# Kernel optimization log

Hardware: AMD Instinct MI355X
Metric: run time of the kernel (lower is better)

## Reference

```python
import jax, jax.numpy as jnp
import numpy as np

B, S, D = 2, 2048, 1024
H, DH = 16, 64  # num_heads, per-head depth (kd//H == vd//H)
NEG = -1e10


def setup_inputs() -> dict:
    key = jax.random.key(0)
    ks = jax.random.split(key, 5)
    scale = 0.02
    return {
        "X": jax.random.normal(ks[0], (B, S, D), dtype=jnp.float32),
        "Wq": jax.random.normal(ks[1], (D, D), dtype=jnp.float32) * scale,
        "Wk": jax.random.normal(ks[2], (D, D), dtype=jnp.float32) * scale,
        "Wv": jax.random.normal(ks[3], (D, D), dtype=jnp.float32) * scale,
        "Wo": jax.random.normal(ks[4], (D, D), dtype=jnp.float32) * scale,
    }


def reference(X, Wq, Wk, Wv, Wo):
    # torch nn.Linear(in,out,bias=False): y = x @ W.T, W is [out,in]
    q = X @ Wq.T  # [B,S,H*DH]
    k = X @ Wk.T
    v = X @ Wv.T
    # split heads -> [B,H,S,DH]
    q = q.reshape(B, S, H, DH).transpose(0, 2, 1, 3) * (DH ** -0.5)
    k = k.reshape(B, S, H, DH).transpose(0, 2, 1, 3)
    v = v.reshape(B, S, H, DH).transpose(0, 2, 1, 3)
    # causal bias: -1e10 on strictly upper triangle (psuedolikelihood=False)
    bias = NEG * jnp.triu(jnp.ones((S, S), dtype=jnp.float32), 1)
    # logits[...,q,k] = q . k
    logits = jnp.einsum("bhkd,bhqd->bhqk", k, q) + bias
    weights = jax.nn.softmax(logits, axis=-1)  # [B,H,S,S]
    out = jnp.einsum("bhqk,bhkd->bhqd", weights, v)
    out = out.transpose(0, 2, 1, 3).reshape(B, S, H * DH)
    return out @ Wo.T  # [B,S,D]
```

## Files before the change

### kernel.cpp

```cpp
#include <hip/hip_runtime.h>
#include <math.h>


typedef _Float16 f16x8 __attribute__((ext_vector_type(8)));
typedef _Float16 f16x4 __attribute__((ext_vector_type(4)));
typedef _Float16 f16x2 __attribute__((ext_vector_type(2)));
typedef __attribute__((ext_vector_type(4))) float f32x4;
typedef __attribute__((ext_vector_type(16))) float f32x16;

#define MFMA16(a, b, c) __builtin_amdgcn_mfma_f32_16x16x32_f16(a, b, c, 0, 0, 0)
#define MFMA32(a, b, c) __builtin_amdgcn_mfma_f32_32x32x16_f16(a, b, c, 0, 0, 0)
#define QSCALE 0.18033688f

__device__ __forceinline__ void async16(const void* g, void* l) {
  __builtin_amdgcn_global_load_lds(
      (const __attribute__((address_space(1))) unsigned int*)g,
      (__attribute__((address_space(3))) unsigned int*)l, 16, 0, 0);
}

__device__ __forceinline__ f16x2 pk2(float x, float y) {
  return __builtin_bit_cast(f16x2, __builtin_amdgcn_cvt_pkrtz(x, y));
}

__device__ __forceinline__ f16x8 cvt8(const float* __restrict__ p) {
  float4 a = *(const float4*)p;
  float4 b = *(const float4*)(p + 4);
  f16x2 p0 = pk2(a.x, a.y), p1 = pk2(a.z, a.w);
  f16x2 p2 = pk2(b.x, b.y), p3 = pk2(b.z, b.w);
  f16x8 h;
  h[0] = p0[0]; h[1] = p0[1]; h[2] = p1[0]; h[3] = p1[1];
  h[4] = p2[0]; h[5] = p2[1]; h[6] = p3[0]; h[7] = p3[1];
  return h;
}

__global__ void convert_all(const float* __restrict__ X, const float* __restrict__ Wq,
                            const float* __restrict__ Wk, const float* __restrict__ Wv,
                            const float* __restrict__ Wo, _Float16* __restrict__ Xh,
                            _Float16* __restrict__ Wqkvh, _Float16* __restrict__ Woh) {
  size_t i = ((size_t)blockIdx.x * 256 + threadIdx.x) * 8;
  const float* src; _Float16* dst; size_t off;
  if (i < 4194304u)      { src = X;  dst = Xh;              off = i; }
  else if (i < 5242880u) { src = Wq; dst = Wqkvh;           off = i - 4194304u; }
  else if (i < 6291456u) { src = Wk; dst = Wqkvh + 1048576; off = i - 5242880u; }
  else if (i < 7340032u) { src = Wv; dst = Wqkvh + 2097152; off = i - 6291456u; }
  else                   { src = Wo; dst = Woh;             off = i - 7340032u; }
  *(f16x8*)(dst + off) = cvt8(src + off);
}

__global__ __launch_bounds__(256) void gemm_qkv_a(
    const _Float16* __restrict__ Xh, const _Float16* __restrict__ Wh,
    _Float16* __restrict__ Qh, _Float16* __restrict__ Kh,
    _Float16* __restrict__ Vth) {
  __shared__ _Float16 As[128 * 32];
  __shared__ _Float16 Bs[128 * 32];
  const int tid = threadIdx.x;
  const int wave = tid >> 6, lane = tid & 63;
  const int quad = lane >> 4, l16 = lane & 15;
  const int wm = (wave >> 1) * 64, wn = (wave & 1) * 64;
  const int bn = blockIdx.x, bm = blockIdx.y;
  const int mat = bn >> 3;

  const int r0 = tid >> 2, cc0 = (tid & 3) * 8;
  const int r1 = (tid + 256) >> 2, cc1 = (tid & 3) * 8;
  const _Float16* gA0 = &Xh[(size_t)(bm * 128 + r0) * 1024 + cc0];
  const _Float16* gA1 = &Xh[(size_t)(bm * 128 + r1) * 1024 + cc1];
  const _Float16* gB0 = &Wh[(size_t)(bn * 128 + r0) * 1024 + cc0];
  const _Float16* gB1 = &Wh[(size_t)(bn * 128 + r1) * 1024 + cc1];

  f32x4 acc[4][4] = {};

  for (int k0 = 0; k0 < 1024; k0 += 32) {
    __syncthreads();
    async16(gA0 + k0, &As[(wave * 64) * 8]);
    async16(gA1 + k0, &As[(256 + wave * 64) * 8]);
    async16(gB0 + k0, &Bs[(wave * 64) * 8]);
    async16(gB1 + k0, &Bs[(256 + wave * 64) * 8]);
    __syncthreads();
    f16x8 af[4], bf[4];
#pragma unroll
    for (int t = 0; t < 4; ++t) {
      af[t] = *(const f16x8*)&As[(wm + t * 16 + l16) * 32 + quad * 8];
      bf[t] = *(const f16x8*)&Bs[(wn + t * 16 + l16) * 32 + quad * 8];
    }
#pragma unroll
    for (int mt = 0; mt < 4; ++mt)
#pragma unroll
      for (int nt = 0; nt < 4; ++nt)
        acc[mt][nt] = MFMA16(af[mt], bf[nt], acc[mt][nt]);
  }

#pragma unroll
  for (int mt = 0; mt < 4; ++mt) {
    int m_base = bm * 128 + wm + mt * 16 + quad * 4;
    int b = m_base >> 11, sb = m_base & 2047;
#pragma unroll
    for (int nt = 0; nt < 4; ++nt) {
      int ob = (bn * 128 + wn + nt * 16) & 1023;
      int h = ob >> 6;
      int dh = (ob & 63) + l16;
      size_t bh = (size_t)(b * 16 + h);
      if (mat == 0) {
#pragma unroll
        for (int r = 0; r < 4; ++r)
          Qh[(bh * 2048 + sb + r) * 64 + dh] = (_Float16)(acc[mt][nt][r] * QSCALE);
      } else if (mat == 1) {
#pragma unroll
        for (int r = 0; r < 4; ++r)
          Kh[(bh * 2048 + sb + r) * 64 + dh] = (_Float16)acc[mt][nt][r];
      } else {
        f16x4 pk;
        pk[0] = (_Float16)acc[mt][nt][0];
        pk[1] = (_Float16)acc[mt][nt][1];
        pk[2] = (_Float16)acc[mt][nt][2];
        pk[3] = (_Float16)acc[mt][nt][3];
        *(f16x4*)&Vth[(bh * 64 + dh) * 2048 + sb] = pk;
      }
    }
  }
}

__global__ __launch_bounds__(256) void gemm_qkv_f(
    const _Float16* __restrict__ Xh, const float* __restrict__ Wq,
    const float* __restrict__ Wk, const float* __restrict__ Wv,
    _Float16* __restrict__ Qh, _Float16* __restrict__ Kh,
    _Float16* __restrict__ Vth) {
  __shared__ _Float16 As[128 * 72];
  __shared__ _Float16 Bs[128 * 72];
  const int tid = threadIdx.x;
  const int wave = tid >> 6, lane = tid & 63;
  const int quad = lane >> 4, l16 = lane & 15;
  const int wm = (wave >> 1) * 64, wn = (wave & 1) * 64;
  const int bn = blockIdx.x, bm = blockIdx.y;
  const int mat = bn >> 3;
  const float* Bsrc = (mat == 0) ? Wq : (mat == 1) ? Wk : Wv;
  const int brow0 = (bn & 7) * 128;

  f32x4 acc[4][4] = {};

  for (int k0 = 0; k0 < 1024; k0 += 64) {
    __syncthreads();
#pragma unroll
    for (int j = 0; j < 4; ++j) {
      int idx = tid + j * 256;
      int row = idx >> 3, c8 = idx & 7;
      *(int4*)&As[row * 72 + c8 * 8] =
          *(const int4*)&Xh[(size_t)(bm * 128 + row) * 1024 + k0 + c8 * 8];
      *(f16x8*)&Bs[row * 72 + c8 * 8] =
          cvt8(&Bsrc[(size_t)(brow0 + row) * 1024 + k0 + c8 * 8]);
    }
    __syncthreads();
#pragma unroll
    for (int kc = 0; kc < 2; ++kc) {
      f16x8 af[4], bf[4];
#pragma unroll
      for (int t = 0; t < 4; ++t) {
        af[t] = *(const f16x8*)&As[(wm + t * 16 + l16) * 72 + kc * 32 + quad * 8];
        bf[t] = *(const f16x8*)&Bs[(wn + t * 16 + l16) * 72 + kc * 32 + quad * 8];
      }
#pragma unroll
      for (int mt = 0; mt < 4; ++mt)
#pragma unroll
        for (int nt = 0; nt < 4; ++nt)
          acc[mt][nt] = MFMA16(af[mt], bf[nt], acc[mt][nt]);
    }
  }

#pragma unroll
  for (int mt = 0; mt < 4; ++mt) {
    int m_base = bm * 128 + wm + mt * 16 + quad * 4;
    int b = m_base >> 11, sb = m_base & 2047;
#pragma unroll
    for (int nt = 0; nt < 4; ++nt) {
      int ob = (bn * 128 + wn + nt * 16) & 1023;
      int h = ob >> 6;
      int dh = (ob & 63) + l16;
      size_t bh = (size_t)(b * 16 + h);
      if (mat == 0) {
#pragma unroll
        for (int r = 0; r < 4; ++r)
          Qh[(bh * 2048 + sb + r) * 64 + dh] = (_Float16)(acc[mt][nt][r] * QSCALE);
      } else if (mat == 1) {
#pragma unroll
        for (int r = 0; r < 4; ++r)
          Kh[(bh * 2048 + sb + r) * 64 + dh] = (_Float16)acc[mt][nt][r];
      } else {
        f16x4 pk;
        pk[0] = (_Float16)acc[mt][nt][0];
        pk[1] = (_Float16)acc[mt][nt][1];
        pk[2] = (_Float16)acc[mt][nt][2];
        pk[3] = (_Float16)acc[mt][nt][3];
        *(f16x4*)&Vth[(bh * 64 + dh) * 2048 + sb] = pk;
      }
    }
  }
}

__global__ __launch_bounds__(512) void attn_kernel(
    const _Float16* __restrict__ Qg, const _Float16* __restrict__ Kg,
    const _Float16* __restrict__ Vtg, _Float16* __restrict__ Og) {
  __shared__ _Float16 smem[2 * (128 * 72 + 64 * 136)];
  const int bh = blockIdx.x;
  const int qt = 15 - (int)blockIdx.y;
  const int q0 = qt * 128;
  const int tid = threadIdx.x;
  const int group = tid >> 8;
  const int tidg = tid & 255;
  const int wv = (tid >> 6) & 3;
  const int lane = tid & 63;
  const int l31 = lane & 31, hl = lane >> 5;
  const int b = bh >> 4, h = bh & 15;
  const int qrow = q0 + wv * 32 + l31;

  _Float16* Kl = smem + group * (128 * 72 + 64 * 136);
  _Float16* Vl = Kl + 128 * 72;

  const _Float16* Qbase = Qg + ((size_t)bh * 2048 + qrow) * 64 + hl * 8;
  f16x8 aq[4];
#pragma unroll
  for (int t = 0; t < 4; ++t) aq[t] = *(const f16x8*)(Qbase + 16 * t);

  f32x16 oacc[2] = {};
  float lsum = 0.f;

  const int nmax = (qt + 2) >> 1;
  for (int it = 0; it < nmax; ++it) {
    const int kt = 2 * it + group;
    const bool valid = (kt <= qt);
    const int k0 = kt << 7;
    __syncthreads();
    if (valid) {
#pragma unroll
      for (int i = tidg; i < 1024; i += 256) {
        int row = i >> 3, c8 = i & 7;
        *(int4*)&Kl[row * 72 + c8 * 8] =
            *(const int4*)&Kg[((size_t)bh * 2048 + k0 + row) * 64 + c8 * 8];
      }
#pragma unroll
      for (int i = tidg; i < 1024; i += 256) {
        int row = i >> 4, c16 = i & 15;
        *(int4*)&Vl[row * 136 + c16 * 8] =
            *(const int4*)&Vtg[((size_t)bh * 64 + row) * 2048 + k0 + c16 * 8];
      }
    }
    __syncthreads();
    if (!valid) continue;

    const bool diag = (kt == qt);

#pragma unroll
    for (int s32t = 0; s32t < 4; ++s32t) {
      f32x16 tv = {};
#pragma unroll
      for (int t = 0; t < 4; ++t) {
        f16x8 kb = *(const f16x8*)&Kl[(s32t * 32 + l31) * 72 + t * 16 + hl * 8];
        tv = MFMA32(kb, aq[t], tv);
      }
      int pkx[8];
#pragma unroll
      for (int i = 0; i < 8; ++i) {
        float x0 = tv[2 * i], x1 = tv[2 * i + 1];
        int kg = k0 + s32t * 32 + ((2 * i) & 3) + 8 * (i >> 1) + 4 * hl;
        if (diag) {
          if (kg > qrow) x0 = -1e30f;
          if (kg + 1 > qrow) x1 = -1e30f;
        }
        x0 = __builtin_amdgcn_exp2f(x0);
        x1 = __builtin_amdgcn_exp2f(x1);
        lsum += x0 + x1;
        pkx[i] = __builtin_bit_cast(int, pk2(x0, x1));
      }
      int s0 = hl ? pkx[0] : pkx[2];
      int s1 = hl ? pkx[1] : pkx[3];
      int s2 = hl ? pkx[4] : pkx[6];
      int s3 = hl ? pkx[5] : pkx[7];
      int r0 = __shfl_xor(s0, 32);
      int r1 = __shfl_xor(s1, 32);
      int r2 = __shfl_xor(s2, 32);
      int r3 = __shfl_xor(s3, 32);
      int4 f0, f1;
      f0.x = hl ? r0 : pkx[0];
      f0.y = hl ? r1 : pkx[1];
      f0.z = hl ? pkx[2] : r0;
      f0.w = hl ? pkx[3] : r1;
      f1.x = hl ? r2 : pkx[4];
      f1.y = hl ? r3 : pkx[5];
      f1.z = hl ? pkx[6] : r2;
      f1.w = hl ? pkx[7] : r3;
      f16x8 bp0 = __builtin_bit_cast(f16x8, f0);
      f16x8 bp1 = __builtin_bit_cast(f16x8, f1);
#pragma unroll
      for (int d = 0; d < 2; ++d) {
        f16x8 vb0 = *(const f16x8*)&Vl[(d * 32 + l31) * 136 + s32t * 32 + hl * 8];
        f16x8 vb1 =
            *(const f16x8*)&Vl[(d * 32 + l31) * 136 + s32t * 32 + 16 + hl * 8];
        oacc[d] = MFMA32(vb0, bp0, oacc[d]);
        oacc[d] = MFMA32(vb1, bp1, oacc[d]);
      }
    }
  }

  __syncthreads();
  float* mbuf = (float*)(smem + (128 * 72 + 64 * 136));
  float* slot = mbuf + (wv * 64 + lane) * 33;
  if (group == 1) {
#pragma unroll
    for (int d = 0; d < 2; ++d)
#pragma unroll
      for (int j = 0; j < 16; ++j) slot[d * 16 + j] = oacc[d][j];
    slot[32] = lsum;
  }
  __syncthreads();
  if (group == 0) {
#pragma unroll
    for (int d = 0; d < 2; ++d)
#pragma unroll
      for (int j = 0; j < 16; ++j) oacc[d][j] += slot[d * 16 + j];
    lsum += slot[32];
    lsum += __shfl_xor(lsum, 32);
    float inv = 1.0f / lsum;
#pragma unroll
    for (int d = 0; d < 2; ++d)
#pragma unroll
      for (int rq = 0; rq < 4; ++rq) {
        f16x4 o;
#pragma unroll
        for (int j = 0; j < 4; ++j)
          o[j] = (_Float16)(oacc[d][rq * 4 + j] * inv);
        int dh = d * 32 + 8 * rq + 4 * hl;
        *(f16x4*)&Og[(((size_t)b * 2048 + qrow) * 16 + h) * 64 + dh] = o;
      }
  }
}

template <int BH>
__global__ __launch_bounds__(256) void gemm_out(
    const _Float16* __restrict__ A, const float* __restrict__ Wo,
    const _Float16* __restrict__ Woh, float* __restrict__ Co) {
  __shared__ _Float16 As[128 * 72];
  __shared__ _Float16 Bs[64 * 72];
  const int tid = threadIdx.x;
  const int wave = tid >> 6, lane = tid & 63;
  const int quad = lane >> 4, l16 = lane & 15;
  const int wm = (wave >> 1) * 64, wn = (wave & 1) * 32;
  const int bn = blockIdx.x, bm = blockIdx.y;

  f32x4 acc[4][2] = {};

  for (int k0 = 0; k0 < 1024; k0 += 64) {
    __syncthreads();
#pragma unroll
    for (int j = 0; j < 4; ++j) {
      int idx = tid + j * 256;
      int row = idx >> 3, c8 = idx & 7;
      *(int4*)&As[row * 72 + c8 * 8] =
          *(const int4*)&A[(size_t)(bm * 128 + row) * 1024 + k0 + c8 * 8];
    }
#pragma unroll
    for (int j = 0; j < 2; ++j) {
      int idx = tid + j * 256;
      int row = idx >> 3, c8 = idx & 7;
      if (BH)
        *(int4*)&Bs[row * 72 + c8 * 8] =
            *(const int4*)&Woh[(size_t)(bn * 64 + row) * 1024 + k0 + c8 * 8];
      else
        *(f16x8*)&Bs[row * 72 + c8 * 8] =
            cvt8(&Wo[(size_t)(bn * 64 + row) * 1024 + k0 + c8 * 8]);
    }
    __syncthreads();
#pragma unroll
    for (int kc = 0; kc < 2; ++kc) {
      f16x8 af[4], bf[2];
#pragma unroll
      for (int t = 0; t < 4; ++t)
        af[t] = *(const f16x8*)&As[(wm + t * 16 + l16) * 72 + kc * 32 + quad * 8];
#pragma unroll
      for (int t = 0; t < 2; ++t)
        bf[t] = *(const f16x8*)&Bs[(wn + t * 16 + l16) * 72 + kc * 32 + quad * 8];
#pragma unroll
      for (int mt = 0; mt < 4; ++mt)
#pragma unroll
        for (int nt = 0; nt < 2; ++nt)
          acc[mt][nt] = MFMA16(af[mt], bf[nt], acc[mt][nt]);
    }
  }

#pragma unroll
  for (int mt = 0; mt < 4; ++mt) {
    int m_base = bm * 128 + wm + mt * 16 + quad * 4;
#pragma unroll
    for (int nt = 0; nt < 2; ++nt) {
      int n = bn * 64 + wn + nt * 16 + l16;
#pragma unroll
      for (int r = 0; r < 4; ++r)
        Co[(size_t)(m_base + r) * 1024 + n] = acc[mt][nt][r];
    }
  }
}

extern "C" void kernel_launch(void* const* d_in, const int* in_sizes, int n_in,
                              void* d_out, int out_size, void* d_ws, size_t ws_size,
                              hipStream_t stream) {
  const float* X  = (const float*)d_in[0];
  const float* Wq = (const float*)d_in[1];
  const float* Wk = (const float*)d_in[2];
  const float* Wv = (const float*)d_in[3];
  const float* Wo = (const float*)d_in[4];
  float* out = (float*)d_out;

  _Float16* Qh    = (_Float16*)d_out;
  _Float16* Kh    = Qh + 4194304;
  _Float16* Vth   = (_Float16*)d_ws;
  _Float16* Xh    = Vth + 4194304;
  _Float16* Og    = Xh;
  _Float16* Wqkvh = Xh + 4194304;
  _Float16* Woh   = Wqkvh + 3145728;

  const bool big = (ws_size >= 25165824u);

  convert_all<<<big ? 4096 : 2048, 256, 0, stream>>>(X, Wq, Wk, Wv, Wo,
                                                     Xh, Wqkvh, Woh);
  if (big)
    gemm_qkv_a<<<dim3(24, 32), 256, 0, stream>>>(Xh, Wqkvh, Qh, Kh, Vth);
  else
    gemm_qkv_f<<<dim3(24, 32), 256, 0, stream>>>(Xh, Wq, Wk, Wv, Qh, Kh, Vth);
  attn_kernel<<<dim3(32, 16), 512, 0, stream>>>(Qh, Kh, Vth, Og);
  if (big)
    gemm_out<1><<<dim3(16, 32), 256, 0, stream>>>(Og, Wo, Woh, out);
  else
    gemm_out<0><<<dim3(16, 32), 256, 0, stream>>>(Og, Wo, nullptr, out);
}
```

Before: 176.6 us.

## Register-prefetch next K/V tiles during attention compute and split row-sum accumulators

The attention loop now loads the next iteration's K and V tiles from global memory into registers while the current tile is being processed. After the barrier, those registers are written to shared memory, which hides global load latency behind the MFMA and exp work. Launch bounds now request 4 waves per SIMD, and the softmax row sum is split into two accumulators to shorten the add dependency chain. The extra 32 registers of prefetch buffer plus the tighter register cap could cause spills or lower occupancy.

```diff
diff --git a/kernel.cpp b/kernel.cpp
--- a/kernel.cpp
+++ b/kernel.cpp
@@ -195,7 +195,7 @@
   }
 }
 
-__global__ __launch_bounds__(512) void attn_kernel(
+__global__ __launch_bounds__(512, 4) void attn_kernel(
     const _Float16* __restrict__ Qg, const _Float16* __restrict__ Kg,
     const _Float16* __restrict__ Vtg, _Float16* __restrict__ Og) {
   __shared__ _Float16 smem[2 * (128 * 72 + 64 * 136)];
@@ -220,7 +220,24 @@
   for (int t = 0; t < 4; ++t) aq[t] = *(const f16x8*)(Qbase + 16 * t);
 
   f32x16 oacc[2] = {};
-  float lsum = 0.f;
+  float la = 0.f, lb = 0.f;
+
+  const int krow = tidg >> 3, kc8 = (tidg & 7) * 8;
+  const int vrow = tidg >> 4, vc16 = (tidg & 15) * 8;
+  const _Float16* gKp =
+      Kg + ((size_t)bh * 2048 + group * 128 + krow) * 64 + kc8;
+  const _Float16* gVp =
+      Vtg + ((size_t)bh * 64 + vrow) * 2048 + group * 128 + vc16;
+
+  int4 pk[4], pv[4];
+  if (group <= qt) {
+#pragma unroll
+    for (int j = 0; j < 4; ++j)
+      pk[j] = *(const int4*)(gKp + (size_t)j * 32 * 64);
+#pragma unroll
+    for (int j = 0; j < 4; ++j)
+      pv[j] = *(const int4*)(gVp + (size_t)j * 16 * 2048);
+  }
 
   const int nmax = (qt + 2) >> 1;
   for (int it = 0; it < nmax; ++it) {
@@ -230,17 +247,21 @@
     __syncthreads();
     if (valid) {
 #pragma unroll
-      for (int i = tidg; i < 1024; i += 256) {
-        int row = i >> 3, c8 = i & 7;
-        *(int4*)&Kl[row * 72 + c8 * 8] =
-            *(const int4*)&Kg[((size_t)bh * 2048 + k0 + row) * 64 + c8 * 8];
-      }
-#pragma unroll
-      for (int i = tidg; i < 1024; i += 256) {
-        int row = i >> 4, c16 = i & 15;
-        *(int4*)&Vl[row * 136 + c16 * 8] =
-            *(const int4*)&Vtg[((size_t)bh * 64 + row) * 2048 + k0 + c16 * 8];
-      }
+      for (int j = 0; j < 4; ++j)
+        *(int4*)&Kl[(krow + j * 32) * 72 + kc8] = pk[j];
+#pragma unroll
+      for (int j = 0; j < 4; ++j)
+        *(int4*)&Vl[(vrow + j * 16) * 136 + vc16] = pv[j];
+    }
+    if (kt + 2 <= qt) {
+      const _Float16* nK = gKp + (size_t)(it + 1) * 256 * 64;
+      const _Float16* nV = gVp + (size_t)(it + 1) * 256;
+#pragma unroll
+      for (int j = 0; j < 4; ++j)
+        pk[j] = *(const int4*)(nK + (size_t)j * 32 * 64);
+#pragma unroll
+      for (int j = 0; j < 4; ++j)
+        pv[j] = *(const int4*)(nV + (size_t)j * 16 * 2048);
     }
     __syncthreads();
     if (!valid) continue;
@@ -266,7 +287,8 @@
         }
         x0 = __builtin_amdgcn_exp2f(x0);
         x1 = __builtin_amdgcn_exp2f(x1);
-        lsum += x0 + x1;
+        la += x0;
+        lb += x1;
         pkx[i] = __builtin_bit_cast(int, pk2(x0, x1));
       }
       int s0 = hl ? pkx[0] : pkx[2];
@@ -299,6 +321,7 @@
     }
   }
 
+  float lsum = la + lb;
   __syncthreads();
   float* mbuf = (float*)(smem + (128 * 72 + 64 * 136));
   float* slot = mbuf + (wv * 64 + lane) * 33;
```

After: 212.0 us. 20.0% more time.

## Prefetch next K/V tiles into registers to overlap global loads with compute

Applied to the files above, without the earlier changes.

Replaces the synchronous global-to-LDS copy of each K/V tile with a register double-buffer. The next tile (kt+2, clamped to qt) is loaded into registers while the current tile is processed, and the staged registers are written to LDS at the top of each iteration. The row-sum accumulator is also split into two independent partial sums to shorten the dependency chain. This costs extra VGPRs (8 int4 held live), which may lower occupancy, and issues redundant loads of the clamped tile on the last iterations.

```diff
diff --git a/kernel.cpp b/kernel.cpp
--- a/kernel.cpp
+++ b/kernel.cpp
@@ -220,7 +220,27 @@
   for (int t = 0; t < 4; ++t) aq[t] = *(const f16x8*)(Qbase + 16 * t);
 
   f32x16 oacc[2] = {};
-  float lsum = 0.f;
+  float la = 0.f, lb = 0.f;
+
+  const int krow = tidg >> 3, kc8 = (tidg & 7) * 8;
+  const int vrow = tidg >> 4, vc16 = (tidg & 15) * 8;
+  const _Float16* gK = Kg + ((size_t)bh * 2048 + krow) * 64 + kc8;
+  const _Float16* gV = Vtg + ((size_t)bh * 64 + vrow) * 2048 + vc16;
+
+  int4 ka0, ka1, ka2, ka3, va0, va1, va2, va3;
+  {
+    const int ktp = (group <= qt) ? group : qt;
+    const _Float16* kp = gK + (size_t)ktp * (128 * 64);
+    const _Float16* vp = gV + (size_t)ktp * 128;
+    ka0 = *(const int4*)(kp + 0 * 32 * 64);
+    ka1 = *(const int4*)(kp + 1 * 32 * 64);
+    ka2 = *(const int4*)(kp + 2 * 32 * 64);
+    ka3 = *(const int4*)(kp + 3 * 32 * 64);
+    va0 = *(const int4*)(vp + 0 * 16 * 2048);
+    va1 = *(const int4*)(vp + 1 * 16 * 2048);
+    va2 = *(const int4*)(vp + 2 * 16 * 2048);
+    va3 = *(const int4*)(vp + 3 * 16 * 2048);
+  }
 
   const int nmax = (qt + 2) >> 1;
   for (int it = 0; it < nmax; ++it) {
@@ -228,19 +248,26 @@
     const bool valid = (kt <= qt);
     const int k0 = kt << 7;
     __syncthreads();
-    if (valid) {
-#pragma unroll
-      for (int i = tidg; i < 1024; i += 256) {
-        int row = i >> 3, c8 = i & 7;
-        *(int4*)&Kl[row * 72 + c8 * 8] =
-            *(const int4*)&Kg[((size_t)bh * 2048 + k0 + row) * 64 + c8 * 8];
-      }
-#pragma unroll
-      for (int i = tidg; i < 1024; i += 256) {
-        int row = i >> 4, c16 = i & 15;
-        *(int4*)&Vl[row * 136 + c16 * 8] =
-            *(const int4*)&Vtg[((size_t)bh * 64 + row) * 2048 + k0 + c16 * 8];
-      }
+    *(int4*)&Kl[(krow + 0) * 72 + kc8] = ka0;
+    *(int4*)&Kl[(krow + 32) * 72 + kc8] = ka1;
+    *(int4*)&Kl[(krow + 64) * 72 + kc8] = ka2;
+    *(int4*)&Kl[(krow + 96) * 72 + kc8] = ka3;
+    *(int4*)&Vl[(vrow + 0) * 136 + vc16] = va0;
+    *(int4*)&Vl[(vrow + 16) * 136 + vc16] = va1;
+    *(int4*)&Vl[(vrow + 32) * 136 + vc16] = va2;
+    *(int4*)&Vl[(vrow + 48) * 136 + vc16] = va3;
+    {
+      const int ktn = (kt + 2 <= qt) ? (kt + 2) : qt;
+      const _Float16* kp = gK + (size_t)ktn * (128 * 64);
+      const _Float16* vp = gV + (size_t)ktn * 128;
+      ka0 = *(const int4*)(kp + 0 * 32 * 64);
+      ka1 = *(const int4*)(kp + 1 * 32 * 64);
+      ka2 = *(const int4*)(kp + 2 * 32 * 64);
+      ka3 = *(const int4*)(kp + 3 * 32 * 64);
+      va0 = *(const int4*)(vp + 0 * 16 * 2048);
+      va1 = *(const int4*)(vp + 1 * 16 * 2048);
+      va2 = *(const int4*)(vp + 2 * 16 * 2048);
+      va3 = *(const int4*)(vp + 3 * 16 * 2048);
     }
     __syncthreads();
     if (!valid) continue;
@@ -266,7 +293,8 @@
         }
         x0 = __builtin_amdgcn_exp2f(x0);
         x1 = __builtin_amdgcn_exp2f(x1);
-        lsum += x0 + x1;
+        la += x0;
+        lb += x1;
         pkx[i] = __builtin_bit_cast(int, pk2(x0, x1));
       }
       int s0 = hl ? pkx[0] : pkx[2];
@@ -299,6 +327,7 @@
     }
   }
 
+  float lsum = la + lb;
   __syncthreads();
   float* mbuf = (float*)(smem + (128 * 72 + 64 * 136));
   float* slot = mbuf + (wv * 64 + lane) * 33;
```

New measurement: 172.6 us (median of 3 runs). 2.3% less time.
